# Kernel optimization log

Hardware: AMD Instinct MI355X
Metric: run time of the kernel (lower is better)

Reference implementation:

```python
import jax, jax.numpy as jnp
import numpy as np

D_DIM = 1024
K_DIM = 16
B, L = 4, 2048

def setup_inputs() -> dict:
    key = jax.random.key(0)
    kx, ky, kz, kw, kb = jax.random.split(key, 5)
    x = jax.random.normal(kx, (B, L, D_DIM), dtype=jnp.float32)
    y = jax.random.normal(ky, (B, L, D_DIM), dtype=jnp.float32)
    z = jax.random.normal(kz, (B, L, D_DIM), dtype=jnp.float32)
    bound = 1.0 / np.sqrt(3 * D_DIM)  # torch Linear init scale
    W = jax.random.uniform(kw, (K_DIM * D_DIM, 3 * D_DIM), dtype=jnp.float32, minval=-bound, maxval=bound)
    b = jax.random.uniform(kb, (K_DIM * D_DIM,), dtype=jnp.float32, minval=-bound, maxval=bound)
    return {"x": x, "y": y, "z": z, "W": W, "b": b}

def reference(x, y, z, W, b):
    Bsz, Lsz, D = x.shape
    inp = jnp.concatenate([x, y, z], axis=-1)                 # (B, L, 3D)
    kernel = jnp.einsum('blc,fc->blf', inp, W) + b            # (B, L, k*D)
    kernel = kernel.reshape(Bsz, Lsz, D, K_DIM)               # (B, L, D, k)
    # einsum 'bldk,bld->bld' == sum over k, then elementwise multiply
    return kernel.sum(axis=-1) * (x * y)
```

## Files before the change

### kernel.cpp

```cpp
#include <hip/hip_runtime.h>

#define M_ROWS 8192
#define N_DIM  1024
#define K3     3072
#define KD     16
#define NKT    48
#define BM     256
#define BN     128
#define BK     64
#define LDS_A  (BM * BK)
#define LDS_B  (BN * BK)
#define LDS_TILE (LDS_A + LDS_B)

typedef __bf16 bf16x8 __attribute__((ext_vector_type(8)));
typedef float  f32x4  __attribute__((ext_vector_type(4)));

__device__ __forceinline__ unsigned short f2bf(float f) {
  return __builtin_bit_cast(unsigned short, (__bf16)f);
}
__device__ __forceinline__ float bf2f(unsigned short u) {
  return __builtin_bit_cast(float, (unsigned int)u << 16);
}
__device__ __forceinline__ ushort4 pack4(float4 f) {
  ushort4 o; o.x = f2bf(f.x); o.y = f2bf(f.y); o.z = f2bf(f.z); o.w = f2bf(f.w);
  return o;
}

__device__ __forceinline__ void async16(const void* g, void* l) {
  __builtin_amdgcn_global_load_lds(
      (const __attribute__((address_space(1))) unsigned int*)g,
      (__attribute__((address_space(3))) unsigned int*)l, 16, 0, 0);
}

__global__ __launch_bounds__(256) void prep_kernel(
    const float4* __restrict__ x, const float4* __restrict__ y, const float4* __restrict__ z,
    const float* __restrict__ W, const float* __restrict__ b,
    ushort4* __restrict__ Ib4, ushort4* __restrict__ P4,
    ushort4* __restrict__ Wsum4, float* __restrict__ bsum)
{
  int bid = blockIdx.x;
  int tid = threadIdx.x;
  if (bid < 8192) {
    int i = bid * 256 + tid;
    int m = bid;
    int c4 = tid;
    float4 fx = x[i], fy = y[i], fz = z[i];
    size_t rb = (size_t)m * 768;
    Ib4[rb + c4]       = pack4(fx);
    Ib4[rb + 256 + c4] = pack4(fy);
    Ib4[rb + 512 + c4] = pack4(fz);
    float4 p; p.x = fx.x * fy.x; p.y = fx.y * fy.y; p.z = fx.z * fy.z; p.w = fx.w * fy.w;
    P4[i] = pack4(p);
  } else if (bid < 11264) {
    int g  = (bid - 8192) * 256 + tid;
    int d  = g / 768;
    int cq = g - d * 768;
    const float4* wrow = (const float4*)(W + (size_t)d * (KD * K3));
    float sx = 0.f, sy = 0.f, sz = 0.f, sw = 0.f;
    #pragma unroll
    for (int k = 0; k < KD; ++k) {
      float4 t = wrow[(size_t)k * (K3 / 4) + cq];
      sx += t.x; sy += t.y; sz += t.z; sw += t.w;
    }
    ushort4 o; o.x = f2bf(sx); o.y = f2bf(sy); o.z = f2bf(sz); o.w = f2bf(sw);
    Wsum4[g] = o;
  } else {
    int d = (bid - 11264) * 256 + tid;
    if (d < N_DIM) {
      float s = 0.f;
      #pragma unroll
      for (int k = 0; k < KD; ++k) s += b[d * KD + k];
      bsum[d] = s;
    }
  }
}

__global__ __launch_bounds__(512, 2) void gemm_ep_kernel(
    const unsigned short* __restrict__ Ib, const unsigned short* __restrict__ Wsum,
    const float* __restrict__ bsum, const unsigned short* __restrict__ P,
    float* __restrict__ out)
{
  extern __shared__ unsigned short lds[];

  int bid = blockIdx.x;
  int swz = (bid & 7) * 32 + (bid >> 3);
  int mt = swz >> 3;
  int nt = swz & 7;
  int m0 = mt * BM, n0 = nt * BN;

  int tid  = threadIdx.x;
  int lane = tid & 63;
  int wid  = tid >> 6;
  int wr = wid >> 1, wc = wid & 1;

  int row0 = tid >> 3;
  int ch0  = tid & 7;
  int dofs = tid * 16;

  const unsigned short* Abase = Ib   + (size_t)m0 * K3;
  const unsigned short* Bbase = Wsum + (size_t)n0 * K3;

  f32x4 acc[4][4];
  #pragma unroll
  for (int i = 0; i < 4; ++i)
    #pragma unroll
    for (int j = 0; j < 4; ++j)
      acc[i][j] = f32x4{0.f, 0.f, 0.f, 0.f};

  int fr = lane & 15;
  int hi = lane >> 4;

  auto STAGE = [&](int s, int t) {
    char* dst = (char*)(lds + s * LDS_TILE);
    int k0 = t << 6;
    #pragma unroll
    for (int r = 0; r < 4; ++r) {
      int row = row0 + r * 64;
      int sc  = ((ch0 ^ (row0 & 7)) << 3);
      async16(Abase + (size_t)row * K3 + k0 + sc, dst + dofs + r * 8192);
    }
    #pragma unroll
    for (int r = 0; r < 2; ++r) {
      int row = row0 + r * 64;
      int sc  = ((ch0 ^ (row0 & 7)) << 3);
      async16(Bbase + (size_t)row * K3 + k0 + sc, dst + 2 * LDS_A + dofs + r * 8192);
    }
  };

  STAGE(0, 0);
  STAGE(1, 1);

  for (int t = 0; t < NKT; ++t) {
    int cur = t % 3;
    if (t + 2 < NKT) {
      STAGE((t + 2) % 3, t + 2);
      asm volatile("s_waitcnt vmcnt(12)" ::: "memory");
    } else if (t + 1 < NKT) {
      asm volatile("s_waitcnt vmcnt(6)" ::: "memory");
    } else {
      asm volatile("s_waitcnt vmcnt(0)" ::: "memory");
    }
    __builtin_amdgcn_s_barrier();

    const unsigned short* pA = lds + cur * LDS_TILE;
    const unsigned short* pB = pA + LDS_A;

    __builtin_amdgcn_s_setprio(1);
    #pragma unroll
    for (int kk = 0; kk < 2; ++kk) {
      bf16x8 a[4], b[4];
      int c = (kk << 2) + hi;
      #pragma unroll
      for (int i = 0; i < 4; ++i) {
        int R = wr * 64 + i * 16 + fr;
        a[i] = *(const bf16x8*)&pA[(R << 6) + ((c ^ (R & 7)) << 3)];
      }
      #pragma unroll
      for (int j = 0; j < 4; ++j) {
        int R = wc * 64 + j * 16 + fr;
        b[j] = *(const bf16x8*)&pB[(R << 6) + ((c ^ (R & 7)) << 3)];
      }
      #pragma unroll
      for (int i = 0; i < 4; ++i)
        #pragma unroll
        for (int j = 0; j < 4; ++j)
          acc[i][j] = __builtin_amdgcn_mfma_f32_16x16x32_bf16(a[i], b[j], acc[i][j], 0, 0, 0);
    }
    __builtin_amdgcn_s_setprio(0);

    asm volatile("s_waitcnt lgkmcnt(0)" ::: "memory");
    __builtin_amdgcn_s_barrier();
  }

  #pragma unroll
  for (int i = 0; i < 4; ++i) {
    #pragma unroll
    for (int j = 0; j < 4; ++j) {
      int n = n0 + wc * 64 + j * 16 + fr;
      float bs = bsum[n];
      #pragma unroll
      for (int r = 0; r < 4; ++r) {
        int m = m0 + wr * 64 + i * 16 + hi * 4 + r;
        size_t idx = (size_t)m * N_DIM + n;
        out[idx] = (acc[i][j][r] + bs) * bf2f(P[idx]);
      }
    }
  }
}

extern "C" void kernel_launch(void* const* d_in, const int* in_sizes, int n_in,
                              void* d_out, int out_size, void* d_ws, size_t ws_size,
                              hipStream_t stream) {
  const float* x = (const float*)d_in[0];
  const float* y = (const float*)d_in[1];
  const float* z = (const float*)d_in[2];
  const float* W = (const float*)d_in[3];
  const float* b = (const float*)d_in[4];
  float* out = (float*)d_out;

  unsigned short* Ib   = (unsigned short*)d_ws;
  unsigned short* Wsum = Ib + (size_t)M_ROWS * K3;
  unsigned short* P    = Wsum + (size_t)N_DIM * K3;
  float*          bsum = (float*)(P + (size_t)M_ROWS * N_DIM);

  prep_kernel<<<11268, 256, 0, stream>>>(
      (const float4*)x, (const float4*)y, (const float4*)z, W, b,
      (ushort4*)Ib, (ushort4*)P, (ushort4*)Wsum, bsum);

  gemm_ep_kernel<<<256, 512, 3 * LDS_TILE * sizeof(unsigned short), stream>>>(
      Ib, Wsum, bsum, P, out);
}
```

Baseline: 140.5 us.

## Split GEMM k-step into two phases interleaving LDS reads, async loads and MFMAs

Restructures the main GEMM loop so each k-tile runs as two half-steps. Each half-step loads LDS fragments, issues part of the next-next tile's global-to-LDS async loads, then runs a block of 16 MFMAs fenced by sched_barrier and workgroup barriers. The aim is to spread global load issue across the compute and keep the matrix cores fed. The cost is more barriers per iteration, and the prologue now waits explicitly for the first tile.

```diff
diff --git a/kernel.cpp b/kernel.cpp
--- a/kernel.cpp
+++ b/kernel.cpp
@@ -96,6 +96,7 @@
   int row0 = tid >> 3;
   int ch0  = tid & 7;
   int dofs = tid * 16;
+  int sc   = ((ch0 ^ (row0 & 7)) << 3);
 
   const unsigned short* Abase = Ib   + (size_t)m0 * K3;
   const unsigned short* Bbase = Wsum + (size_t)n0 * K3;
@@ -110,65 +111,70 @@
   int fr = lane & 15;
   int hi = lane >> 4;
 
-  auto STAGE = [&](int s, int t) {
+  auto STAGE_A = [&](int s, int t, int rlo, int rhi) {
     char* dst = (char*)(lds + s * LDS_TILE);
     int k0 = t << 6;
-    #pragma unroll
-    for (int r = 0; r < 4; ++r) {
-      int row = row0 + r * 64;
-      int sc  = ((ch0 ^ (row0 & 7)) << 3);
-      async16(Abase + (size_t)row * K3 + k0 + sc, dst + dofs + r * 8192);
-    }
-    #pragma unroll
-    for (int r = 0; r < 2; ++r) {
-      int row = row0 + r * 64;
-      int sc  = ((ch0 ^ (row0 & 7)) << 3);
-      async16(Bbase + (size_t)row * K3 + k0 + sc, dst + 2 * LDS_A + dofs + r * 8192);
-    }
-  };
-
-  STAGE(0, 0);
-  STAGE(1, 1);
+    for (int r = rlo; r < rhi; ++r)
+      async16(Abase + (size_t)(row0 + r * 64) * K3 + k0 + sc, dst + dofs + r * 8192);
+  };
+  auto STAGE_B = [&](int s, int t, int rlo, int rhi) {
+    char* dst = (char*)(lds + s * LDS_TILE) + 2 * LDS_A;
+    int k0 = t << 6;
+    for (int r = rlo; r < rhi; ++r)
+      async16(Bbase + (size_t)(row0 + r * 64) * K3 + k0 + sc, dst + dofs + r * 8192);
+  };
+
+  bf16x8 a[4], b[4];
+  auto LOADAB = [&](const unsigned short* pA, const unsigned short* pB, int kk) {
+    int c = (kk << 2) + hi;
+    #pragma unroll
+    for (int i = 0; i < 4; ++i) {
+      int R = wr * 64 + i * 16 + fr;
+      a[i] = *(const bf16x8*)&pA[(R << 6) + ((c ^ (R & 7)) << 3)];
+    }
+    #pragma unroll
+    for (int j = 0; j < 4; ++j) {
+      int R = wc * 64 + j * 16 + fr;
+      b[j] = *(const bf16x8*)&pB[(R << 6) + ((c ^ (R & 7)) << 3)];
+    }
+  };
+  auto MFMA16 = [&]() {
+    __builtin_amdgcn_s_setprio(1);
+    #pragma unroll
+    for (int i = 0; i < 4; ++i)
+      #pragma unroll
+      for (int j = 0; j < 4; ++j)
+        acc[i][j] = __builtin_amdgcn_mfma_f32_16x16x32_bf16(a[i], b[j], acc[i][j], 0, 0, 0);
+    __builtin_amdgcn_s_setprio(0);
+  };
+
+  STAGE_A(0, 0, 0, 4); STAGE_B(0, 0, 0, 2);
+  STAGE_A(1, 1, 0, 4); STAGE_B(1, 1, 0, 2);
+  asm volatile("s_waitcnt vmcnt(6)" ::: "memory");
+  __builtin_amdgcn_s_barrier();
 
   for (int t = 0; t < NKT; ++t) {
-    int cur = t % 3;
-    if (t + 2 < NKT) {
-      STAGE((t + 2) % 3, t + 2);
-      asm volatile("s_waitcnt vmcnt(12)" ::: "memory");
-    } else if (t + 1 < NKT) {
-      asm volatile("s_waitcnt vmcnt(6)" ::: "memory");
-    } else {
-      asm volatile("s_waitcnt vmcnt(0)" ::: "memory");
-    }
-    __builtin_amdgcn_s_barrier();
-
-    const unsigned short* pA = lds + cur * LDS_TILE;
+    const unsigned short* pA = lds + (t % 3) * LDS_TILE;
     const unsigned short* pB = pA + LDS_A;
-
-    __builtin_amdgcn_s_setprio(1);
-    #pragma unroll
-    for (int kk = 0; kk < 2; ++kk) {
-      bf16x8 a[4], b[4];
-      int c = (kk << 2) + hi;
-      #pragma unroll
-      for (int i = 0; i < 4; ++i) {
-        int R = wr * 64 + i * 16 + fr;
-        a[i] = *(const bf16x8*)&pA[(R << 6) + ((c ^ (R & 7)) << 3)];
-      }
-      #pragma unroll
-      for (int j = 0; j < 4; ++j) {
-        int R = wc * 64 + j * 16 + fr;
-        b[j] = *(const bf16x8*)&pB[(R << 6) + ((c ^ (R & 7)) << 3)];
-      }
-      #pragma unroll
-      for (int i = 0; i < 4; ++i)
-        #pragma unroll
-        for (int j = 0; j < 4; ++j)
-          acc[i][j] = __builtin_amdgcn_mfma_f32_16x16x32_bf16(a[i], b[j], acc[i][j], 0, 0, 0);
-    }
-    __builtin_amdgcn_s_setprio(0);
-
+    int s2 = (t + 2) % 3;
+    bool st = (t + 2) < NKT;
+
+    LOADAB(pA, pB, 0);
+    if (st) STAGE_A(s2, t + 2, 0, 3);
+    __builtin_amdgcn_s_barrier();
     asm volatile("s_waitcnt lgkmcnt(0)" ::: "memory");
+    __builtin_amdgcn_sched_barrier(0);
+    MFMA16();
+    __builtin_amdgcn_s_barrier();
+
+    LOADAB(pA, pB, 1);
+    if (st) { STAGE_A(s2, t + 2, 3, 4); STAGE_B(s2, t + 2, 0, 2); }
+    if (st) asm volatile("s_waitcnt vmcnt(6)" ::: "memory");
+    else    asm volatile("s_waitcnt vmcnt(0)" ::: "memory");
+    __builtin_amdgcn_s_barrier();
+    asm volatile("s_waitcnt lgkmcnt(0)" ::: "memory");
+    __builtin_amdgcn_sched_barrier(0);
+    MFMA16();
     __builtin_amdgcn_s_barrier();
   }
 
```

After: 130.4 us. 1.08x faster.

## Load B operand directly to registers and double-buffer A with larger K tiles

Applied to the files above, without the earlier changes.

The GEMM main loop is restructured. The B (Wsum) fragments are now loaded straight from global memory into registers, prefetched one tile ahead and double-buffered in registers, and only A goes through LDS. BK doubles to 128, the LDS pipeline drops from three stages to two, and the A staging is split into two halves interleaved with the MFMA work using sched_barrier and tuned vmcnt waits. The aim is to cut LDS traffic and barrier count per K step. In exchange it takes more VGPRs for the B buffers, and the loads go straight to global memory without LDS reuse across waves.

```diff
diff --git a/kernel.cpp b/kernel.cpp
--- a/kernel.cpp
+++ b/kernel.cpp
@@ -4,13 +4,11 @@
 #define N_DIM  1024
 #define K3     3072
 #define KD     16
-#define NKT    48
 #define BM     256
 #define BN     128
-#define BK     64
+#define BK     128
+#define NKT    24
 #define LDS_A  (BM * BK)
-#define LDS_B  (BN * BK)
-#define LDS_TILE (LDS_A + LDS_B)
 
 typedef __bf16 bf16x8 __attribute__((ext_vector_type(8)));
 typedef float  f32x4  __attribute__((ext_vector_type(4)));
@@ -92,13 +90,20 @@
   int lane = tid & 63;
   int wid  = tid >> 6;
   int wr = wid >> 1, wc = wid & 1;
-
-  int row0 = tid >> 3;
-  int ch0  = tid & 7;
+  int fr = lane & 15;
+  int hi = lane >> 4;
+
+  int row0 = tid >> 4;
+  int ch0  = tid & 15;
+  int sc   = (ch0 ^ (row0 & 15)) << 3;
   int dofs = tid * 16;
 
-  const unsigned short* Abase = Ib   + (size_t)m0 * K3;
-  const unsigned short* Bbase = Wsum + (size_t)n0 * K3;
+  const unsigned short* Abase = Ib + (size_t)m0 * K3;
+
+  int bb[4];
+  #pragma unroll
+  for (int j = 0; j < 4; ++j)
+    bb[j] = (n0 + wc * 64 + j * 16 + fr) * K3 + hi * 8;
 
   f32x4 acc[4][4];
   #pragma unroll
@@ -107,69 +112,75 @@
     for (int j = 0; j < 4; ++j)
       acc[i][j] = f32x4{0.f, 0.f, 0.f, 0.f};
 
-  int fr = lane & 15;
-  int hi = lane >> 4;
-
-  auto STAGE = [&](int s, int t) {
-    char* dst = (char*)(lds + s * LDS_TILE);
-    int k0 = t << 6;
-    #pragma unroll
-    for (int r = 0; r < 4; ++r) {
-      int row = row0 + r * 64;
-      int sc  = ((ch0 ^ (row0 & 7)) << 3);
-      async16(Abase + (size_t)row * K3 + k0 + sc, dst + dofs + r * 8192);
-    }
-    #pragma unroll
-    for (int r = 0; r < 2; ++r) {
-      int row = row0 + r * 64;
-      int sc  = ((ch0 ^ (row0 & 7)) << 3);
-      async16(Bbase + (size_t)row * K3 + k0 + sc, dst + 2 * LDS_A + dofs + r * 8192);
-    }
-  };
-
-  STAGE(0, 0);
-  STAGE(1, 1);
-
-  for (int t = 0; t < NKT; ++t) {
-    int cur = t % 3;
-    if (t + 2 < NKT) {
-      STAGE((t + 2) % 3, t + 2);
-      asm volatile("s_waitcnt vmcnt(12)" ::: "memory");
-    } else if (t + 1 < NKT) {
-      asm volatile("s_waitcnt vmcnt(6)" ::: "memory");
-    } else {
-      asm volatile("s_waitcnt vmcnt(0)" ::: "memory");
-    }
+  auto STAGE_A4 = [&](int slot, int t, int rlo) {
+    char* dst = (char*)lds + slot * (LDS_A * 2);
+    int k0 = t * BK;
+    #pragma unroll
+    for (int r = rlo; r < rlo + 4; ++r)
+      async16(Abase + (size_t)(row0 + r * 32) * K3 + k0 + sc, dst + dofs + r * 8192);
+  };
+  auto LOADB8 = [&](int t, int kkb, bf16x8* dst) {
+    int k0 = t * BK + kkb * 32;
+    #pragma unroll
+    for (int q = 0; q < 8; ++q) {
+      int kk = q >> 2, j = q & 3;
+      dst[q] = *(const bf16x8*)&Wsum[(size_t)(bb[j] + k0 + kk * 32)];
+    }
+  };
+  auto LOADA = [&](const unsigned short* pA, int kk, bf16x8* a) {
+    #pragma unroll
+    for (int i = 0; i < 4; ++i) {
+      int R = wr * 64 + i * 16 + fr;
+      a[i] = *(const bf16x8*)&pA[R * BK + ((((kk << 2) + hi) ^ fr) << 3)];
+    }
+  };
+  auto MF = [&](bf16x8* a, bf16x8* b4) {
+    __builtin_amdgcn_s_setprio(1);
+    #pragma unroll
+    for (int i = 0; i < 4; ++i)
+      #pragma unroll
+      for (int j = 0; j < 4; ++j)
+        acc[i][j] = __builtin_amdgcn_mfma_f32_16x16x32_bf16(a[i], b4[j], acc[i][j], 0, 0, 0);
+    __builtin_amdgcn_s_setprio(0);
+  };
+
+  bf16x8 bE0[8], bL0[8], bE1[8], bL1[8];
+
+  auto TILE = [&](int t, int slot, bf16x8* bEc, bf16x8* bLc, bf16x8* bEn, bf16x8* bLn, bool st) {
+    const unsigned short* pA = lds + slot * LDS_A;
+    bf16x8 a[4];
+    LOADA(pA, 0, a);
+    if (st) { LOADB8(t + 1, 0, bEn); STAGE_A4(slot ^ 1, t + 1, 0); }
+    MF(a, bEc + 0);
+    LOADA(pA, 1, a);
+    MF(a, bEc + 4);
     __builtin_amdgcn_s_barrier();
-
-    const unsigned short* pA = lds + cur * LDS_TILE;
-    const unsigned short* pB = pA + LDS_A;
-
-    __builtin_amdgcn_s_setprio(1);
-    #pragma unroll
-    for (int kk = 0; kk < 2; ++kk) {
-      bf16x8 a[4], b[4];
-      int c = (kk << 2) + hi;
-      #pragma unroll
-      for (int i = 0; i < 4; ++i) {
-        int R = wr * 64 + i * 16 + fr;
-        a[i] = *(const bf16x8*)&pA[(R << 6) + ((c ^ (R & 7)) << 3)];
-      }
-      #pragma unroll
-      for (int j = 0; j < 4; ++j) {
-        int R = wc * 64 + j * 16 + fr;
-        b[j] = *(const bf16x8*)&pB[(R << 6) + ((c ^ (R & 7)) << 3)];
-      }
-      #pragma unroll
-      for (int i = 0; i < 4; ++i)
-        #pragma unroll
-        for (int j = 0; j < 4; ++j)
-          acc[i][j] = __builtin_amdgcn_mfma_f32_16x16x32_bf16(a[i], b[j], acc[i][j], 0, 0, 0);
-    }
-    __builtin_amdgcn_s_setprio(0);
-
-    asm volatile("s_waitcnt lgkmcnt(0)" ::: "memory");
+    LOADA(pA, 2, a);
+    if (st) {
+      STAGE_A4(slot ^ 1, t + 1, 4);
+      __builtin_amdgcn_sched_barrier(0x38F);
+      LOADB8(t + 1, 2, bLn);
+    }
+    MF(a, bLc + 0);
+    LOADA(pA, 3, a);
+    MF(a, bLc + 4);
+    if (st) asm volatile("s_waitcnt vmcnt(8)" ::: "memory");
+    else    asm volatile("s_waitcnt vmcnt(0)" ::: "memory");
     __builtin_amdgcn_s_barrier();
+  };
+
+  LOADB8(0, 0, bE0);
+  STAGE_A4(0, 0, 0);
+  STAGE_A4(0, 0, 4);
+  __builtin_amdgcn_sched_barrier(0x38F);
+  LOADB8(0, 2, bL0);
+  asm volatile("s_waitcnt vmcnt(8)" ::: "memory");
+  __builtin_amdgcn_s_barrier();
+
+  #pragma unroll 1
+  for (int th = 0; th < NKT; th += 2) {
+    TILE(th,     0, bE0, bL0, bE1, bL1, true);
+    TILE(th + 1, 1, bE1, bL1, bE0, bL0, th + 2 < NKT);
   }
 
   #pragma unroll
@@ -207,6 +218,6 @@
       (const float4*)x, (const float4*)y, (const float4*)z, W, b,
       (ushort4*)Ib, (ushort4*)P, (ushort4*)Wsum, bsum);
 
-  gemm_ep_kernel<<<256, 512, 3 * LDS_TILE * sizeof(unsigned short), stream>>>(
+  gemm_ep_kernel<<<256, 512, 2 * LDS_A * sizeof(unsigned short), stream>>>(
       Ib, Wsum, bsum, P, out);
 }
```

Measured after the change: 209.9 us. 49.3% more time.

## Restructure GEMM main loop to a single barrier with prefetched LDS fragments

Applied to the files above, without the earlier changes.

Moves the main-loop barrier so each K iteration has one barrier instead of two. All LDS fragment reads for both K halves are issued before the next global-to-LDS stage is launched. MFMAs on the first half start after a partial lgkmcnt wait, so LDS reads overlap with matrix math. The block-index swizzle is dropped for a plain row-major tile mapping, which can change L2 reuse across concurrently running blocks.

```diff
diff --git a/kernel.cpp b/kernel.cpp
--- a/kernel.cpp
+++ b/kernel.cpp
@@ -83,19 +83,21 @@
   extern __shared__ unsigned short lds[];
 
   int bid = blockIdx.x;
-  int swz = (bid & 7) * 32 + (bid >> 3);
-  int mt = swz >> 3;
-  int nt = swz & 7;
+  int mt = bid >> 3;
+  int nt = bid & 7;
   int m0 = mt * BM, n0 = nt * BN;
 
   int tid  = threadIdx.x;
   int lane = tid & 63;
   int wid  = tid >> 6;
   int wr = wid >> 1, wc = wid & 1;
+  int fr = lane & 15;
+  int hi = lane >> 4;
 
   int row0 = tid >> 3;
   int ch0  = tid & 7;
   int dofs = tid * 16;
+  int sc   = (ch0 ^ (row0 & 7)) << 3;
 
   const unsigned short* Abase = Ib   + (size_t)m0 * K3;
   const unsigned short* Bbase = Wsum + (size_t)n0 * K3;
@@ -107,68 +109,73 @@
     for (int j = 0; j < 4; ++j)
       acc[i][j] = f32x4{0.f, 0.f, 0.f, 0.f};
 
-  int fr = lane & 15;
-  int hi = lane >> 4;
-
-  auto STAGE = [&](int s, int t) {
-    char* dst = (char*)(lds + s * LDS_TILE);
+  auto STAGE = [&](int slot, int t) {
+    char* dst = (char*)(lds + slot * LDS_TILE);
     int k0 = t << 6;
     #pragma unroll
-    for (int r = 0; r < 4; ++r) {
-      int row = row0 + r * 64;
-      int sc  = ((ch0 ^ (row0 & 7)) << 3);
-      async16(Abase + (size_t)row * K3 + k0 + sc, dst + dofs + r * 8192);
-    }
-    #pragma unroll
-    for (int r = 0; r < 2; ++r) {
-      int row = row0 + r * 64;
-      int sc  = ((ch0 ^ (row0 & 7)) << 3);
-      async16(Bbase + (size_t)row * K3 + k0 + sc, dst + 2 * LDS_A + dofs + r * 8192);
-    }
+    for (int r = 0; r < 4; ++r)
+      async16(Abase + (size_t)(row0 + r * 64) * K3 + k0 + sc, dst + dofs + r * 8192);
+    char* dstB = dst + 2 * LDS_A;
+    #pragma unroll
+    for (int r = 0; r < 2; ++r)
+      async16(Bbase + (size_t)(row0 + r * 64) * K3 + k0 + sc, dstB + dofs + r * 8192);
+  };
+
+  auto MFMA16 = [&](bf16x8* a, bf16x8* b4) {
+    __builtin_amdgcn_s_setprio(1);
+    #pragma unroll
+    for (int i = 0; i < 4; ++i)
+      #pragma unroll
+      for (int j = 0; j < 4; ++j)
+        acc[i][j] = __builtin_amdgcn_mfma_f32_16x16x32_bf16(a[i], b4[j], acc[i][j], 0, 0, 0);
+    __builtin_amdgcn_s_setprio(0);
   };
 
   STAGE(0, 0);
   STAGE(1, 1);
-
+  asm volatile("s_waitcnt vmcnt(6)" ::: "memory");
+  __builtin_amdgcn_s_barrier();
+
+  #pragma unroll 1
   for (int t = 0; t < NKT; ++t) {
-    int cur = t % 3;
-    if (t + 2 < NKT) {
-      STAGE((t + 2) % 3, t + 2);
-      asm volatile("s_waitcnt vmcnt(12)" ::: "memory");
-    } else if (t + 1 < NKT) {
-      asm volatile("s_waitcnt vmcnt(6)" ::: "memory");
-    } else {
-      asm volatile("s_waitcnt vmcnt(0)" ::: "memory");
-    }
-    __builtin_amdgcn_s_barrier();
-
-    const unsigned short* pA = lds + cur * LDS_TILE;
+    const unsigned short* pA = lds + (t % 3) * LDS_TILE;
     const unsigned short* pB = pA + LDS_A;
-
-    __builtin_amdgcn_s_setprio(1);
-    #pragma unroll
-    for (int kk = 0; kk < 2; ++kk) {
-      bf16x8 a[4], b[4];
-      int c = (kk << 2) + hi;
-      #pragma unroll
-      for (int i = 0; i < 4; ++i) {
-        int R = wr * 64 + i * 16 + fr;
-        a[i] = *(const bf16x8*)&pA[(R << 6) + ((c ^ (R & 7)) << 3)];
-      }
-      #pragma unroll
-      for (int j = 0; j < 4; ++j) {
-        int R = wc * 64 + j * 16 + fr;
-        b[j] = *(const bf16x8*)&pB[(R << 6) + ((c ^ (R & 7)) << 3)];
-      }
-      #pragma unroll
-      for (int i = 0; i < 4; ++i)
-        #pragma unroll
-        for (int j = 0; j < 4; ++j)
-          acc[i][j] = __builtin_amdgcn_mfma_f32_16x16x32_bf16(a[i], b[j], acc[i][j], 0, 0, 0);
-    }
-    __builtin_amdgcn_s_setprio(0);
-
+    bool st = (t + 2) < NKT;
+
+    bf16x8 a[2][4], b[2][4];
+    #pragma unroll
+    for (int i = 0; i < 4; ++i) {
+      int R = wr * 64 + i * 16 + fr;
+      a[0][i] = *(const bf16x8*)&pA[(R << 6) + (((hi) ^ (R & 7)) << 3)];
+    }
+    #pragma unroll
+    for (int j = 0; j < 4; ++j) {
+      int R = wc * 64 + j * 16 + fr;
+      b[0][j] = *(const bf16x8*)&pB[(R << 6) + (((hi) ^ (R & 7)) << 3)];
+    }
+    __builtin_amdgcn_sched_barrier(0);
+    #pragma unroll
+    for (int i = 0; i < 4; ++i) {
+      int R = wr * 64 + i * 16 + fr;
+      a[1][i] = *(const bf16x8*)&pA[(R << 6) + (((4 + hi) ^ (R & 7)) << 3)];
+    }
+    #pragma unroll
+    for (int j = 0; j < 4; ++j) {
+      int R = wc * 64 + j * 16 + fr;
+      b[1][j] = *(const bf16x8*)&pB[(R << 6) + (((4 + hi) ^ (R & 7)) << 3)];
+    }
+    if (st) STAGE((t + 2) % 3, t + 2);
+    __builtin_amdgcn_sched_barrier(0);
+
+    asm volatile("s_waitcnt lgkmcnt(8)" ::: "memory");
+    __builtin_amdgcn_sched_barrier(0);
+    MFMA16(a[0], b[0]);
     asm volatile("s_waitcnt lgkmcnt(0)" ::: "memory");
+    __builtin_amdgcn_sched_barrier(0);
+    MFMA16(a[1], b[1]);
+
+    if (st) asm volatile("s_waitcnt vmcnt(6)" ::: "memory");
+    else    asm volatile("s_waitcnt vmcnt(0)" ::: "memory");
     __builtin_amdgcn_s_barrier();
   }
 
```

Result: no change. 138.3 us (-1.6%).
